# Kernel optimization log

Measured on AMD Instinct MI355X. Metric: run time of the kernel, lower is better.

Reference implementation:

```python
import jax, jax.numpy as jnp
import numpy as np

T, B, DIM = 64, 16, 512
H, Dh, ETA = 8, 64, 4
FD = ETA * Dh  # feature_dim = 256
EPS = 1e-6


def setup_inputs() -> dict:
    key = jax.random.key(0)
    ks = jax.random.split(key, 12)

    def w(k, o, i):
        return jax.random.normal(k, (o, i), jnp.float32) * (1.0 / np.sqrt(i).astype(np.float32))

    return {
        "inputs": jax.random.normal(ks[0], (T, B, DIM), jnp.float32),
        "terminations": jax.random.randint(ks[1], (T, B), 0, 2).astype(jnp.int32),
        "kv_state_prev": jnp.zeros((B, H, FD, Dh), jnp.float32),
        "norm_state_prev": jnp.zeros((B, H, FD), jnp.float32),
        "Wq": w(ks[2], H * Dh, DIM),
        "Wk": w(ks[3], H * Dh, DIM),
        "Wv": w(ks[4], H * Dh, DIM),
        "Wb": w(ks[5], H * Dh, DIM),
        "Wg": w(ks[6], H * Dh, DIM),
        "Wp1": w(ks[7], H * ETA, DIM),
        "Wp2": w(ks[8], H * ETA, DIM),
        "Wp3": w(ks[9], H * ETA, DIM),
        "Wo": w(ks[10], DIM, H * Dh),
        "bo": jnp.zeros((DIM,), jnp.float32),
    }


def reference(inputs, terminations, kv_state_prev, norm_state_prev,
              Wq, Wk, Wv, Wb, Wg, Wp1, Wp2, Wp3, Wo, bo):
    def proj(W, e):
        return (inputs @ W.T).reshape(T, B, H, e)

    q = proj(Wq, Dh)
    k = proj(Wk, Dh)
    v = proj(Wv, Dh)
    beta = jax.nn.sigmoid(proj(Wb, Dh))
    gamma = jax.nn.sigmoid(proj(Wg, Dh))
    p1 = proj(Wp1, ETA)
    p2 = proj(Wp2, ETA)
    p3 = proj(Wp3, ETA)

    # feature map: outer product of relu(p) [eta] and x [head_dim] -> [eta*head_dim]
    def fmap(x, p):
        return jnp.einsum('tbhe,tbhd->tbhed', jax.nn.relu(p), x).reshape(T, B, H, FD)

    phi_q = fmap(q, p2)
    psi_k = fmap(k, p1)
    # gamma map: outer product of sigmoid(p3) and sigmoid-gated gamma, values in (0,1)
    gamma_feat = jnp.einsum('tbhe,tbhd->tbhed', jax.nn.sigmoid(p3), gamma).reshape(T, B, H, FD)

    gated_v = v * beta                       # [T,B,H,Dh]
    gated_k = psi_k * gamma_feat             # [T,B,H,FD]

    term_mask = (1.0 - terminations.astype(jnp.float32))[:, :, None, None]  # [T,B,1,1]
    discount = (1.0 - gamma_feat) * term_mask  # [T,B,H,FD]

    kv_upd = jnp.einsum('tbhd,tbhD->tbhDd', gated_v, gated_k)  # [T,B,H,FD,Dh]

    def step(carry, x):
        kv, nm = carry
        d, u_kv, u_nm = x
        kv = d[..., None] * kv + u_kv
        nm = d * nm + u_nm
        return (kv, nm), (kv, nm)

    _, (kv_all, nm_all) = jax.lax.scan(step, (kv_state_prev, norm_state_prev),
                                       (discount, kv_upd, gated_k))

    attn_num = jnp.einsum('tbhDd,tbhD->tbhd', kv_all, phi_q)
    attn_den = jnp.einsum('tbhD,tbhD->tbh', phi_q, nm_all)
    attn_out = (attn_num / (attn_den[..., None] + EPS)).reshape(T, B, H * Dh)
    output = attn_out @ Wo.T + bo
    return (output, kv_all[-1], nm_all[-1])
```

## Files before the change

kernel.cpp:

```cpp
#include <hip/hip_runtime.h>


#define T_N   64
#define B_N   16
#define DIM_N 512
#define H_N   8
#define DH_N  64

#define OUT_ELEMS   524288
#define KV_ELEMS    2097152
#define PROJ_ELEMS  2719744

typedef _Float16 f16;
typedef f16   f16x8 __attribute__((ext_vector_type(8)));
typedef float f32x4 __attribute__((ext_vector_type(4)));

__device__ __forceinline__ float sigmoidf_(float x) {
    return 1.0f / (1.0f + __expf(-x));
}

__device__ __forceinline__ void gemm64_core(const float* __restrict__ A,
                                            const float* __restrict__ W,
                                            const float* __restrict__ bias,
                                            float* __restrict__ C, int N,
                                            int mb, int nb, int kBase, int kLen) {
    const int nbase = nb * 64;
    if (nbase >= N) return;

    __shared__ float As[2][16][68];
    __shared__ float Bs[2][16][68];

    const int tid = threadIdx.x;
    const int mbase = mb * 64;
    const int tx = tid & 15;
    const int ty = tid >> 4;
    const int sr = tid >> 2;
    const int sk = (tid & 3) << 2;
    const bool wok = (nbase + sr) < N;

    const float* Ap = A + (size_t)(mbase + sr) * 512 + kBase + sk;
    const float* Wp = W + (size_t)(nbase + sr) * 512 + kBase + sk;

    float4 av = *(const float4*)Ap;
    float4 wv = wok ? *(const float4*)Wp : make_float4(0.f, 0.f, 0.f, 0.f);
    As[0][sk + 0][sr] = av.x; As[0][sk + 1][sr] = av.y;
    As[0][sk + 2][sr] = av.z; As[0][sk + 3][sr] = av.w;
    Bs[0][sk + 0][sr] = wv.x; Bs[0][sk + 1][sr] = wv.y;
    Bs[0][sk + 2][sr] = wv.z; Bs[0][sk + 3][sr] = wv.w;

    float acc[4][4];
    #pragma unroll
    for (int i = 0; i < 4; ++i)
        #pragma unroll
        for (int j = 0; j < 4; ++j) acc[i][j] = 0.f;

    for (int k0 = 0; k0 < kLen; k0 += 16) {
        const int buf = (k0 >> 4) & 1;
        __syncthreads();
        const bool more = (k0 + 16) < kLen;
        if (more) {
            av = *(const float4*)(Ap + k0 + 16);
            wv = wok ? *(const float4*)(Wp + k0 + 16) : make_float4(0.f, 0.f, 0.f, 0.f);
        }
        #pragma unroll
        for (int k = 0; k < 16; ++k) {
            float4 a  = *(const float4*)&As[buf][k][ty << 2];
            float4 bq = *(const float4*)&Bs[buf][k][tx << 2];
            float ar[4] = {a.x, a.y, a.z, a.w};
            float br[4] = {bq.x, bq.y, bq.z, bq.w};
            #pragma unroll
            for (int i = 0; i < 4; ++i)
                #pragma unroll
                for (int j = 0; j < 4; ++j)
                    acc[i][j] = fmaf(ar[i], br[j], acc[i][j]);
        }
        if (more) {
            const int nbuf = buf ^ 1;
            As[nbuf][sk + 0][sr] = av.x; As[nbuf][sk + 1][sr] = av.y;
            As[nbuf][sk + 2][sr] = av.z; As[nbuf][sk + 3][sr] = av.w;
            Bs[nbuf][sk + 0][sr] = wv.x; Bs[nbuf][sk + 1][sr] = wv.y;
            Bs[nbuf][sk + 2][sr] = wv.z; Bs[nbuf][sk + 3][sr] = wv.w;
        }
    }

    #pragma unroll
    for (int i = 0; i < 4; ++i) {
        const int m = mbase + (ty << 2) + i;
        #pragma unroll
        for (int j = 0; j < 4; ++j) {
            const int n = nbase + (tx << 2) + j;
            if (n < N) {
                float v = acc[i][j];
                if (bias) v += bias[n];
                C[(size_t)m * N + n] = v;
            }
        }
    }
}

struct ProjW {
    const float* W[8];
    float*       D[8];
};

__device__ __forceinline__ void cvt_split_store(f16* __restrict__ dh,
                                                f16* __restrict__ dl,
                                                float4 v0, float4 v1) {
    float x[8] = {v0.x, v0.y, v0.z, v0.w, v1.x, v1.y, v1.z, v1.w};
    f16x8 h, lo;
    #pragma unroll
    for (int e = 0; e < 8; ++e) {
        f16 hh = (f16)x[e];
        h[e]  = hh;
        lo[e] = (f16)(x[e] - (float)hh);
    }
    *(f16x8*)dh = h;
    *(f16x8*)dl = lo;
}

__global__ __launch_bounds__(256) void proj_mfma_kernel(const float* __restrict__ X,
                                                        ProjW a) {
    const int id = blockIdx.x;
    const int z = id & 7;
    const int rem = id >> 3;
    const int mb = rem & 15;
    const int nb = rem >> 4;
    const int N = (z < 5) ? 512 : 32;
    const int nbase = nb * 64;
    if (nbase >= N) return;

    const float* __restrict__ W = a.W[z];
    float* __restrict__ C = a.D[z];
    const int mbase = mb * 64;

    __shared__ f16 AsH[2][64][40];
    __shared__ f16 AsL[2][64][40];
    __shared__ f16 BsH[2][64][40];
    __shared__ f16 BsL[2][64][40];

    const int tid = threadIdx.x;
    const int sr = tid >> 2;
    const int kq = (tid & 3) << 3;
    const bool wok = (nbase + sr) < N;
    const float* Ap = X + (size_t)(mbase + sr) * 512 + kq;
    const float* Wp = W + (size_t)(nbase + sr) * 512 + kq;

    const int l  = tid & 63;
    const int w  = tid >> 6;
    const int wr = (w >> 1) << 5;
    const int wc = (w & 1) << 5;
    const int lr = l & 15;
    const int lk = (l >> 4) << 3;

    f32x4 acc[2][2] = {};

    float4 xa0 = *(const float4*)(Ap);
    float4 xa1 = *(const float4*)(Ap + 4);
    float4 wb0 = wok ? *(const float4*)(Wp)     : make_float4(0.f, 0.f, 0.f, 0.f);
    float4 wb1 = wok ? *(const float4*)(Wp + 4) : make_float4(0.f, 0.f, 0.f, 0.f);
    cvt_split_store(&AsH[0][sr][kq], &AsL[0][sr][kq], xa0, xa1);
    cvt_split_store(&BsH[0][sr][kq], &BsL[0][sr][kq], wb0, wb1);

    for (int k0 = 0; k0 < 512; k0 += 32) {
        const int buf = (k0 >> 5) & 1;
        __syncthreads();
        const bool more = (k0 + 32) < 512;
        if (more) {
            xa0 = *(const float4*)(Ap + k0 + 32);
            xa1 = *(const float4*)(Ap + k0 + 36);
            wb0 = wok ? *(const float4*)(Wp + k0 + 32) : make_float4(0.f, 0.f, 0.f, 0.f);
            wb1 = wok ? *(const float4*)(Wp + k0 + 36) : make_float4(0.f, 0.f, 0.f, 0.f);
        }

        f16x8 aH[2], aL[2], bH[2], bL[2];
        #pragma unroll
        for (int i = 0; i < 2; ++i) {
            const int row = wr + i * 16 + lr;
            aH[i] = *(const f16x8*)&AsH[buf][row][lk];
            aL[i] = *(const f16x8*)&AsL[buf][row][lk];
        }
        #pragma unroll
        for (int j = 0; j < 2; ++j) {
            const int col = wc + j * 16 + lr;
            bH[j] = *(const f16x8*)&BsH[buf][col][lk];
            bL[j] = *(const f16x8*)&BsL[buf][col][lk];
        }

        #pragma unroll
        for (int i = 0; i < 2; ++i)
            #pragma unroll
            for (int j = 0; j < 2; ++j) {
                acc[i][j] = __builtin_amdgcn_mfma_f32_16x16x32_f16(aH[i], bH[j], acc[i][j], 0, 0, 0);
                acc[i][j] = __builtin_amdgcn_mfma_f32_16x16x32_f16(aH[i], bL[j], acc[i][j], 0, 0, 0);
                acc[i][j] = __builtin_amdgcn_mfma_f32_16x16x32_f16(aL[i], bH[j], acc[i][j], 0, 0, 0);
            }

        if (more) {
            const int nbuf = buf ^ 1;
            cvt_split_store(&AsH[nbuf][sr][kq], &AsL[nbuf][sr][kq], xa0, xa1);
            cvt_split_store(&BsH[nbuf][sr][kq], &BsL[nbuf][sr][kq], wb0, wb1);
        }
    }

    #pragma unroll
    for (int j = 0; j < 2; ++j) {
        const int n = nbase + wc + j * 16 + lr;
        if (n < N) {
            #pragma unroll
            for (int i = 0; i < 2; ++i) {
                #pragma unroll
                for (int q = 0; q < 4; ++q) {
                    const int m = mbase + wr + i * 16 + ((l >> 4) << 2) + q;
                    C[(size_t)m * N + n] = acc[i][j][q];
                }
            }
        }
    }
}

__global__ __launch_bounds__(256) void out_gemm_kernel(const float* __restrict__ A,
                                                       const float* __restrict__ W,
                                                       const float* __restrict__ bias,
                                                       float* __restrict__ C) {
    gemm64_core(A, W, bias, C, 512, blockIdx.x, blockIdx.y, 0, 512);
}

struct OutP { float* P[4]; };
__global__ __launch_bounds__(256) void out_partial_kernel(const float* __restrict__ A,
                                                          const float* __restrict__ W,
                                                          OutP p) {
    const int id = blockIdx.x;
    const int m = id & 15;
    const int n = (id >> 4) & 7;
    const int kq = id >> 7;
    gemm64_core(A, W, nullptr, p.P[kq], 512, m, n, kq * 128, 128);
}

__global__ __launch_bounds__(256) void out_reduce_kernel(
    const float* __restrict__ p0, const float* __restrict__ p1,
    const float* __restrict__ p2, const float* __restrict__ p3,
    const float* __restrict__ bias, float* __restrict__ out) {
    const int i = blockIdx.x * 256 + threadIdx.x;
    float4 a = ((const float4*)p0)[i];
    float4 b = ((const float4*)p1)[i];
    float4 c = ((const float4*)p2)[i];
    float4 d = ((const float4*)p3)[i];
    float4 bv = ((const float4*)bias)[i & 127];
    float4 r;
    r.x = a.x + b.x + c.x + d.x + bv.x;
    r.y = a.y + b.y + c.y + d.y + bv.y;
    r.z = a.z + b.z + c.z + d.z + bv.z;
    r.w = a.w + b.w + c.w + d.w + bv.w;
    ((float4*)out)[i] = r;
}

__global__ __launch_bounds__(256) void gate_kernel(
    const float* __restrict__ qb,  const float* __restrict__ kb,
    const float* __restrict__ vb,  const float* __restrict__ bb,
    const float* __restrict__ gb,  const float* __restrict__ p1b,
    const float* __restrict__ p2b, const float* __restrict__ p3b,
    const int* __restrict__ term,
    float* __restrict__ disc_g, float* __restrict__ gk_g,
    float* __restrict__ phiq_g, float* __restrict__ gv_g) {
    const int h = blockIdx.x;
    const int row = blockIdx.y;
    const int D = threadIdx.x;
    const int e = D >> 6, di = D & 63;
    const size_t base = (size_t)row * 512 + h * 64;
    const size_t pb = (size_t)row * 32 + h * 4;

    float q = qb[base + di], k = kb[base + di], g = gb[base + di];
    float p1 = p1b[pb + e], p2 = p2b[pb + e], p3 = p3b[pb + e];
    float mask = 1.0f - (float)term[row];
    float gf = sigmoidf_(p3) * sigmoidf_(g);

    const size_t o = ((size_t)row * 8 + h) * 256 + D;
    disc_g[o] = (1.0f - gf) * mask;
    gk_g[o]   = fmaxf(p1, 0.f) * k * gf;
    phiq_g[o] = fmaxf(p2, 0.f) * q;
    if (D < 64)
        gv_g[((size_t)row * 8 + h) * 64 + D] = vb[base + D] * sigmoidf_(bb[base + D]);
}

#define LOADG(P, tt) do { \
    const size_t go_ = (size_t)(tt) * 32768 + gbase; \
    P##d0 = *(const float4*)(disc_g + go_); P##d1 = *(const float4*)(disc_g + go_ + 4); \
    P##g0 = *(const float4*)(gk_g + go_);   P##g1 = *(const float4*)(gk_g + go_ + 4); \
    P##p0 = *(const float4*)(phiq_g + go_); P##p1 = *(const float4*)(phiq_g + go_ + 4); \
    P##gv = *(const float2*)(gv_g + (size_t)(tt) * 8192 + gvb); \
} while (0)

#define STEPC(P, tt) do { \
    const float dj[8]  = {P##d0.x, P##d0.y, P##d0.z, P##d0.w, P##d1.x, P##d1.y, P##d1.z, P##d1.w}; \
    const float gkj[8] = {P##g0.x, P##g0.y, P##g0.z, P##g0.w, P##g1.x, P##g1.y, P##g1.z, P##g1.w}; \
    const float phj[8] = {P##p0.x, P##p0.y, P##p0.z, P##p0.w, P##p1.x, P##p1.y, P##p1.z, P##p1.w}; \
    const float gvx = P##gv.x, gvy = P##gv.y; \
    if ((tt) + 2 < T_N) LOADG(P, (tt) + 2); \
    float den = 0.f, n0 = 0.f, n1 = 0.f; \
    _Pragma("unroll") \
    for (int j = 0; j < 8; ++j) { \
        nm[j] = dj[j] * nm[j] + gkj[j]; \
        den = fmaf(phj[j], nm[j], den); \
        kv[j][0] = dj[j] * kv[j][0] + gkj[j] * gvx; n0 = fmaf(phj[j], kv[j][0], n0); \
        kv[j][1] = dj[j] * kv[j][1] + gkj[j] * gvy; n1 = fmaf(phj[j], kv[j][1], n1); \
    } \
    _Pragma("unroll") \
    for (int ofs = 1; ofs <= 16; ofs <<= 1) { \
        n0 += __shfl_xor(n0, ofs); n1 += __shfl_xor(n1, ofs); den += __shfl_xor(den, ofs); \
    } \
    if (li == 0) { \
        const size_t vbo = (size_t)((tt) * B_N + b) * 512 + h * 64 + d0; \
        vb[vbo]     = n0 / (den + 1e-6f); \
        vb[vbo + 1] = n1 / (den + 1e-6f); \
    } \
} while (0)

__global__ __launch_bounds__(256) void scan7_kernel(
    const float* __restrict__ disc_g, const float* __restrict__ gk_g,
    const float* __restrict__ phiq_g, const float* __restrict__ gv_g,
    float* __restrict__ vb ,
    const float* __restrict__ kv0, const float* __restrict__ nm0,
    float* __restrict__ dout) {
    const int blk = blockIdx.x;
    const int bh = blk & 127;
    const int s  = blk >> 7;
    const int b  = bh >> 3;
    const int h  = bh & 7;
    const int tid = threadIdx.x;
    const int w = tid >> 6;
    const int l = tid & 63;
    const int half = l >> 5;
    const int li = l & 31;
    const int d0 = s * 16 + w * 4 + half * 2;
    const int D0 = li << 3;

    const size_t gbase = ((size_t)b * 8 + h) * 256 + D0;
    const size_t gvb   = ((size_t)b * 8 + h) * 64 + d0;

    float kv[8][2];
    float nm[8];
    {
        const float* kp = kv0 + ((size_t)bh * 256 + D0) * 64 + d0;
        #pragma unroll
        for (int j = 0; j < 8; ++j) {
            float2 r = *(const float2*)(kp + (size_t)j * 64);
            kv[j][0] = r.x; kv[j][1] = r.y;
        }
        float4 na  = *(const float4*)(nm0 + (size_t)bh * 256 + D0);
        float4 nb_ = *(const float4*)(nm0 + (size_t)bh * 256 + D0 + 4);
        nm[0] = na.x; nm[1] = na.y; nm[2] = na.z; nm[3] = na.w;
        nm[4] = nb_.x; nm[5] = nb_.y; nm[6] = nb_.z; nm[7] = nb_.w;
    }

    float4 Ad0, Ad1, Ag0, Ag1, Ap0, Ap1; float2 Agv;
    float4 Bd0, Bd1, Bg0, Bg1, Bp0, Bp1; float2 Bgv;
    LOADG(A, 0);
    LOADG(B, 1);

    for (int t = 0; t < T_N; t += 2) {
        STEPC(A, t);
        STEPC(B, t + 1);
    }

    {
        float* kp = dout + OUT_ELEMS + ((size_t)bh * 256 + D0) * 64 + d0;
        #pragma unroll
        for (int j = 0; j < 8; ++j)
            *(float2*)(kp + (size_t)j * 64) = make_float2(kv[j][0], kv[j][1]);
        if (s == 0 && w == 0 && half == 0) {
            float* np = dout + OUT_ELEMS + KV_ELEMS + (size_t)bh * 256 + D0;
            *(float4*)np       = make_float4(nm[0], nm[1], nm[2], nm[3]);
            *(float4*)(np + 4) = make_float4(nm[4], nm[5], nm[6], nm[7]);
        }
    }
}

extern "C" void kernel_launch(void* const* d_in, const int* in_sizes, int n_in,
                              void* d_out, int out_size, void* d_ws, size_t ws_size,
                              hipStream_t stream) {
    (void)in_sizes; (void)n_in; (void)out_size;

    const float* X    = (const float*)d_in[0];
    const int*   term = (const int*)  d_in[1];
    const float* kv0  = (const float*)d_in[2];
    const float* nm0  = (const float*)d_in[3];
    const float* Wo   = (const float*)d_in[12];
    const float* bo   = (const float*)d_in[13];

    float* out = (float*)d_out;

    float* qb  = (float*)d_ws;
    float* kb  = qb  + 524288;
    float* vb  = kb  + 524288;
    float* bb  = vb  + 524288;
    float* gb  = bb  + 524288;
    float* p1b = gb  + 524288;
    float* p2b = p1b + 32768;
    float* p3b = p2b + 32768;
    float* disc_g = p3b + 32768;
    float* gk_g   = disc_g + 2097152;
    float* phiq_g = gk_g   + 2097152;
    float* gv_g   = phiq_g + 2097152;
    const size_t need_bytes = (size_t)(PROJ_ELEMS + 6815744) * 4;
    const bool big = ws_size >= need_bytes;

    ProjW pa;
    pa.W[0] = (const float*)d_in[4];  pa.W[1] = (const float*)d_in[5];
    pa.W[2] = (const float*)d_in[6];  pa.W[3] = (const float*)d_in[7];
    pa.W[4] = (const float*)d_in[8];  pa.W[5] = (const float*)d_in[9];
    pa.W[6] = (const float*)d_in[10]; pa.W[7] = (const float*)d_in[11];
    pa.D[0] = qb;  pa.D[1] = kb;  pa.D[2] = vb;  pa.D[3] = bb;
    pa.D[4] = gb;  pa.D[5] = p1b; pa.D[6] = p2b; pa.D[7] = p3b;
    proj_mfma_kernel<<<1024, 256, 0, stream>>>(X, pa);

    gate_kernel<<<dim3(8, 1024), 256, 0, stream>>>(qb, kb, vb, bb, gb,
                                                   p1b, p2b, p3b, term,
                                                   disc_g, gk_g, phiq_g, gv_g);
    scan7_kernel<<<512, 256, 0, stream>>>(disc_g, gk_g, phiq_g, gv_g,
                                          vb, kv0, nm0, out);
    if (big) {
        OutP op; op.P[0] = qb; op.P[1] = kb; op.P[2] = bb; op.P[3] = gb;
        out_partial_kernel<<<512, 256, 0, stream>>>(vb, Wo, op);
        out_reduce_kernel<<<512, 256, 0, stream>>>(qb, kb, bb, gb, bo, out);
    } else {
        out_gemm_kernel<<<dim3(16, 8), 256, 0, stream>>>(vb, Wo, bo, out);
    }
}
```

Measured before the change: 190.9 us.

## Split scan across more blocks with full-wave D partition and DPP reductions

New measurement: 188.6 us. About the same (-1.2%).

```diff
diff --git a/kernel.cpp b/kernel.cpp
--- a/kernel.cpp
+++ b/kernel.cpp
@@ -17,6 +17,21 @@
 
 __device__ __forceinline__ float sigmoidf_(float x) {
     return 1.0f / (1.0f + __expf(-x));
+}
+
+template <int CTRL, int RM>
+__device__ __forceinline__ float dpp_add_(float x) {
+    int mv = __builtin_amdgcn_update_dpp(__float_as_int(x), __float_as_int(x),
+                                         CTRL, RM, 0xF, false);
+    return x + __int_as_float(mv);
+}
+__device__ __forceinline__ float half_reduce_dpp(float x) {
+    x = dpp_add_<0xB1, 0xF>(x);
+    x = dpp_add_<0x4E, 0xF>(x);
+    x = dpp_add_<0x141, 0xF>(x);
+    x = dpp_add_<0x140, 0xF>(x);
+    x = dpp_add_<0x142, 0xA>(x);
+    return x;
 }
 
 __device__ __forceinline__ void gemm64_core(const float* __restrict__ A,
@@ -282,40 +297,42 @@
         gv_g[((size_t)row * 8 + h) * 64 + D] = vb[base + D] * sigmoidf_(bb[base + D]);
 }
 
-#define LOADG(P, tt) do { \
-    const size_t go_ = (size_t)(tt) * 32768 + gbase; \
-    P##d0 = *(const float4*)(disc_g + go_); P##d1 = *(const float4*)(disc_g + go_ + 4); \
-    P##g0 = *(const float4*)(gk_g + go_);   P##g1 = *(const float4*)(gk_g + go_ + 4); \
-    P##p0 = *(const float4*)(phiq_g + go_); P##p1 = *(const float4*)(phiq_g + go_ + 4); \
-    P##gv = *(const float2*)(gv_g + (size_t)(tt) * 8192 + gvb); \
+#define LOADT(P, tt) do { \
+    P##d = *(const float4*)(dp + (size_t)(tt) * 32768); \
+    P##g = *(const float4*)(gp + (size_t)(tt) * 32768); \
+    P##q = *(const float4*)(qp + (size_t)(tt) * 32768); \
+    P##v = *(const float2*)(vp + (size_t)(tt) * 8192); \
 } while (0)
 
-#define STEPC(P, tt) do { \
-    const float dj[8]  = {P##d0.x, P##d0.y, P##d0.z, P##d0.w, P##d1.x, P##d1.y, P##d1.z, P##d1.w}; \
-    const float gkj[8] = {P##g0.x, P##g0.y, P##g0.z, P##g0.w, P##g1.x, P##g1.y, P##g1.z, P##g1.w}; \
-    const float phj[8] = {P##p0.x, P##p0.y, P##p0.z, P##p0.w, P##p1.x, P##p1.y, P##p1.z, P##p1.w}; \
-    const float gvx = P##gv.x, gvy = P##gv.y; \
-    if ((tt) + 2 < T_N) LOADG(P, (tt) + 2); \
+#define STEPX(P, Q, tt) do { \
+    if ((tt) + 1 < T_N) LOADT(Q, (tt) + 1); \
     float den = 0.f, n0 = 0.f, n1 = 0.f; \
-    _Pragma("unroll") \
-    for (int j = 0; j < 8; ++j) { \
-        nm[j] = dj[j] * nm[j] + gkj[j]; \
-        den = fmaf(phj[j], nm[j], den); \
-        kv[j][0] = dj[j] * kv[j][0] + gkj[j] * gvx; n0 = fmaf(phj[j], kv[j][0], n0); \
-        kv[j][1] = dj[j] * kv[j][1] + gkj[j] * gvy; n1 = fmaf(phj[j], kv[j][1], n1); \
+    { \
+        const float dj[4] = {P##d.x, P##d.y, P##d.z, P##d.w}; \
+        const float gj[4] = {P##g.x, P##g.y, P##g.z, P##g.w}; \
+        const float qj[4] = {P##q.x, P##q.y, P##q.z, P##q.w}; \
+        const float gvx = P##v.x, gvy = P##v.y; \
+        _Pragma("unroll") \
+        for (int j = 0; j < 4; ++j) { \
+            nm[j] = dj[j] * nm[j] + gj[j]; \
+            den = fmaf(qj[j], nm[j], den); \
+            kv[j][0] = dj[j] * kv[j][0] + gj[j] * gvx; n0 = fmaf(qj[j], kv[j][0], n0); \
+            kv[j][1] = dj[j] * kv[j][1] + gj[j] * gvy; n1 = fmaf(qj[j], kv[j][1], n1); \
+        } \
     } \
-    _Pragma("unroll") \
-    for (int ofs = 1; ofs <= 16; ofs <<= 1) { \
-        n0 += __shfl_xor(n0, ofs); n1 += __shfl_xor(n1, ofs); den += __shfl_xor(den, ofs); \
-    } \
-    if (li == 0) { \
-        const size_t vbo = (size_t)((tt) * B_N + b) * 512 + h * 64 + d0; \
-        vb[vbo]     = n0 / (den + 1e-6f); \
-        vb[vbo + 1] = n1 / (den + 1e-6f); \
+    n0  = half_reduce_dpp(n0); \
+    n1  = half_reduce_dpp(n1); \
+    den = half_reduce_dpp(den); \
+    n0  += __shfl_xor(n0, 32); \
+    n1  += __shfl_xor(n1, 32); \
+    den += __shfl_xor(den, 32); \
+    if (l == 16) { \
+        *(float2*)(vb + (size_t)((tt) * B_N + b) * 512 + h * 64 + d0) = \
+            make_float2(n0 / (den + 1e-6f), n1 / (den + 1e-6f)); \
     } \
 } while (0)
 
-__global__ __launch_bounds__(256) void scan7_kernel(
+__global__ __launch_bounds__(256, 4) void scan10_kernel(
     const float* __restrict__ disc_g, const float* __restrict__ gk_g,
     const float* __restrict__ phiq_g, const float* __restrict__ gv_g,
     float* __restrict__ vb ,
@@ -329,48 +346,45 @@
     const int tid = threadIdx.x;
     const int w = tid >> 6;
     const int l = tid & 63;
-    const int half = l >> 5;
-    const int li = l & 31;
-    const int d0 = s * 16 + w * 4 + half * 2;
-    const int D0 = li << 3;
-
-    const size_t gbase = ((size_t)b * 8 + h) * 256 + D0;
-    const size_t gvb   = ((size_t)b * 8 + h) * 64 + d0;
-
-    float kv[8][2];
-    float nm[8];
+    const int d0 = s * 8 + w * 2;
+    const int D0 = l << 2;
+
+    float kv[4][2];
+    float nm[4];
     {
         const float* kp = kv0 + ((size_t)bh * 256 + D0) * 64 + d0;
         #pragma unroll
-        for (int j = 0; j < 8; ++j) {
+        for (int j = 0; j < 4; ++j) {
             float2 r = *(const float2*)(kp + (size_t)j * 64);
             kv[j][0] = r.x; kv[j][1] = r.y;
         }
-        float4 na  = *(const float4*)(nm0 + (size_t)bh * 256 + D0);
-        float4 nb_ = *(const float4*)(nm0 + (size_t)bh * 256 + D0 + 4);
+        float4 na = *(const float4*)(nm0 + (size_t)bh * 256 + D0);
         nm[0] = na.x; nm[1] = na.y; nm[2] = na.z; nm[3] = na.w;
-        nm[4] = nb_.x; nm[5] = nb_.y; nm[6] = nb_.z; nm[7] = nb_.w;
-    }
-
-    float4 Ad0, Ad1, Ag0, Ag1, Ap0, Ap1; float2 Agv;
-    float4 Bd0, Bd1, Bg0, Bg1, Bp0, Bp1; float2 Bgv;
-    LOADG(A, 0);
-    LOADG(B, 1);
+    }
+
+    const size_t gbase = ((size_t)b * 8 + h) * 256 + D0;
+    const float* dp = disc_g + gbase;
+    const float* gp = gk_g + gbase;
+    const float* qp = phiq_g + gbase;
+    const float* vp = gv_g + ((size_t)b * 8 + h) * 64 + d0;
+
+    float4 Ad, Ag, Aq; float2 Av;
+    float4 Bd, Bg, Bq; float2 Bv;
+    LOADT(A, 0);
 
     for (int t = 0; t < T_N; t += 2) {
-        STEPC(A, t);
-        STEPC(B, t + 1);
+        STEPX(A, B, t);
+        STEPX(B, A, t + 1);
     }
 
     {
         float* kp = dout + OUT_ELEMS + ((size_t)bh * 256 + D0) * 64 + d0;
         #pragma unroll
-        for (int j = 0; j < 8; ++j)
+        for (int j = 0; j < 4; ++j)
             *(float2*)(kp + (size_t)j * 64) = make_float2(kv[j][0], kv[j][1]);
-        if (s == 0 && w == 0 && half == 0) {
+        if (s == 0 && w == 0) {
             float* np = dout + OUT_ELEMS + KV_ELEMS + (size_t)bh * 256 + D0;
-            *(float4*)np       = make_float4(nm[0], nm[1], nm[2], nm[3]);
-            *(float4*)(np + 4) = make_float4(nm[4], nm[5], nm[6], nm[7]);
+            *(float4*)np = make_float4(nm[0], nm[1], nm[2], nm[3]);
         }
     }
 }
@@ -416,8 +430,8 @@
     gate_kernel<<<dim3(8, 1024), 256, 0, stream>>>(qb, kb, vb, bb, gb,
                                                    p1b, p2b, p3b, term,
                                                    disc_g, gk_g, phiq_g, gv_g);
-    scan7_kernel<<<512, 256, 0, stream>>>(disc_g, gk_g, phiq_g, gv_g,
-                                          vb, kv0, nm0, out);
+    scan10_kernel<<<1024, 256, 0, stream>>>(disc_g, gk_g, phiq_g, gv_g,
+                                            vb, kv0, nm0, out);
     if (big) {
         OutP op; op.P[0] = qb; op.P[1] = kb; op.P[2] = bb; op.P[3] = gb;
         out_partial_kernel<<<512, 256, 0, stream>>>(vb, Wo, op);
```
